# Optimization experiments

Measured on AMD Instinct MI355X. Metric: run time of the kernel, lower is better.

Reference implementation:

```python
import jax, jax.numpy as jnp
import numpy as np

B, S, D = 2, 512, 64

def setup_inputs() -> dict:
    key = jax.random.key(0)
    k1, k2, k3, k4, k5 = jax.random.split(key, 5)
    x = jax.random.normal(k1, (B, S, D, D), dtype=jnp.float32)
    log_A = jax.random.normal(k2, (D,), dtype=jnp.float32) * 0.02
    # nn.Linear(dim, 1): weight (1, dim) -> store as (dim,), bias scalar
    dt_w = jax.random.normal(k3, (D,), dtype=jnp.float32) * (1.0 / np.sqrt(D))
    dt_b = jax.random.normal(k4, (), dtype=jnp.float32) * (1.0 / np.sqrt(D))
    # LayerNorm over normalized_shape=(dim, dim)
    ln_w = jnp.ones((D, D), dtype=jnp.float32)
    ln_b = jnp.zeros((D, D), dtype=jnp.float32)
    return {"x": x, "log_A": log_A, "dt_w": dt_w, "dt_b": dt_b, "ln_w": ln_w, "ln_b": ln_b}

def _layernorm_2d(x, w, b, eps=1e-5):
    # normalize over last two dims (d, d)
    mu = jnp.mean(x, axis=(-2, -1), keepdims=True)
    var = jnp.var(x, axis=(-2, -1), keepdims=True)
    return (x - mu) * jax.lax.rsqrt(var + eps) * w + b

def reference(x, log_A, dt_w, dt_b, ln_w, ln_b):
    b, seq, d, _ = x.shape
    x_in = x
    xn = _layernorm_2d(x, ln_w, ln_b)                      # (b, s, d, d)
    A_cont = -jnp.exp(log_A)                               # (d,)
    dt = jax.nn.softplus(jnp.einsum('bsdc,c->bsd', xn, dt_w) + dt_b)  # (b, s, d)
    log_A_dt = dt * A_cont                                 # (b, s, d)
    cs = jnp.cumsum(log_A_dt, axis=1)                      # (b, s, d)
    log_M = cs[:, :, None, :] - cs[:, None, :, :]          # (b, t, j, d)
    idx = jnp.arange(seq)
    mask = (idx[:, None] >= idx[None, :])[None, :, :, None]  # causal (1, t, j, 1)
    M = jnp.exp(jnp.where(mask, log_M, -jnp.inf))          # (b, t, j, d)
    out = jnp.einsum('btjr,bjrc->btrc', M, xn)             # (b, t, d, d)
    return out + x_in
```

## Files before the change

### kernel.cpp

```cpp
#include <hip/hip_runtime.h>
#include <math.h>

#define BB 2
#define SS 512
#define DD 64
#define DDDD 4096
#define NC 32
#define CL (SS / NC)

__global__ __launch_bounds__(256) void k1_stats(
    const float* __restrict__ x, const float* __restrict__ log_A,
    const float* __restrict__ dt_w, const float* __restrict__ dt_b,
    const float* __restrict__ ln_w, const float* __restrict__ ln_b,
    float* __restrict__ a_out, float2* __restrict__ stats)
{
    const int bs  = blockIdx.x;
    const int tid = threadIdx.x;

    const float4* xp4 = (const float4*)(x + (size_t)bs * DDDD + tid * 16);
    float4 v0 = xp4[0], v1 = xp4[1], v2 = xp4[2], v3 = xp4[3];

    float sum = (v0.x+v0.y+v0.z+v0.w) + (v1.x+v1.y+v1.z+v1.w)
              + (v2.x+v2.y+v2.z+v2.w) + (v3.x+v3.y+v3.z+v3.w);
    float sq  = (v0.x*v0.x+v0.y*v0.y+v0.z*v0.z+v0.w*v0.w)
              + (v1.x*v1.x+v1.y*v1.y+v1.z*v1.z+v1.w*v1.w)
              + (v2.x*v2.x+v2.y*v2.y+v2.z*v2.z+v2.w*v2.w)
              + (v3.x*v3.x+v3.y*v3.y+v3.z*v3.z+v3.w*v3.w);

    #pragma unroll
    for (int off = 32; off > 0; off >>= 1) {
        sum += __shfl_down(sum, off);
        sq  += __shfl_down(sq,  off);
    }
    __shared__ float s_sum[4], s_sq[4];
    const int wv = tid >> 6, ln = tid & 63;
    if (ln == 0) { s_sum[wv] = sum; s_sq[wv] = sq; }
    __syncthreads();
    const float tsum = s_sum[0] + s_sum[1] + s_sum[2] + s_sum[3];
    const float tsq  = s_sq[0]  + s_sq[1]  + s_sq[2]  + s_sq[3];
    const float mu   = tsum * (1.0f / DDDD);
    const float var  = tsq  * (1.0f / DDDD) - mu * mu;
    const float rstd = rsqrtf(var + 1e-5f);

    const float4* lw4 = (const float4*)(ln_w + tid * 16);
    const float4* lb4 = (const float4*)(ln_b + tid * 16);
    const float4* dw4 = (const float4*)(dt_w + (tid & 3) * 16);
    float p = 0.f;
    #define ACC4(vv, ii) { \
        float4 lw = lw4[ii], lb = lb4[ii], dw = dw4[ii];            \
        p = fmaf(fmaf((vv.x - mu) * rstd, lw.x, lb.x), dw.x, p);    \
        p = fmaf(fmaf((vv.y - mu) * rstd, lw.y, lb.y), dw.y, p);    \
        p = fmaf(fmaf((vv.z - mu) * rstd, lw.z, lb.z), dw.z, p);    \
        p = fmaf(fmaf((vv.w - mu) * rstd, lw.w, lb.w), dw.w, p);    \
    }
    ACC4(v0, 0); ACC4(v1, 1); ACC4(v2, 2); ACC4(v3, 3);
    #undef ACC4

    p += __shfl_xor(p, 1);
    p += __shfl_xor(p, 2);

    if ((tid & 3) == 0) {
        const int d = tid >> 2;
        float z = p + dt_b[0];
        float dt = (z > 20.f) ? z : log1pf(expf(z));
        float la = dt * (-expf(log_A[d]));
        a_out[bs * DD + d] = expf(la);
    }
    if (tid == 0) stats[bs] = make_float2(mu, rstd);
}

__global__ __launch_bounds__(256) void k2a_partial(
    const float* __restrict__ x, const float* __restrict__ a_in,
    const float* __restrict__ ln_w, const float* __restrict__ ln_b,
    const float2* __restrict__ stats,
    float* __restrict__ Fbuf, float* __restrict__ Pbuf)
{
    const int gw = blockIdx.x * 4 + (threadIdx.x >> 6);
    const int c  = threadIdx.x & 63;
    const int ch = gw & (NC - 1);
    const int br = gw >> 5;
    const int b  = br >> 6, r = br & 63;

    const float lnw = ln_w[r * DD + c];
    const float lnb = ln_b[r * DD + c];

    const int t0 = ch * CL;
    const float*  xp = x + (((size_t)(b * SS + t0)) * DD + r) * DD + c;
    const float*  ap = a_in + (b * SS + t0) * DD + r;
    const float2* sp = stats + b * SS + t0;

    float state = 0.f, P = 1.f;
    #pragma unroll
    for (int t = 0; t < CL; t += 8) {
        float xv[8], av[8]; float2 st[8];
        #pragma unroll
        for (int i = 0; i < 8; ++i) {
            xv[i] = xp[(size_t)(t + i) * DDDD];
            av[i] = ap[(t + i) * DD];
            st[i] = sp[t + i];
        }
        #pragma unroll
        for (int i = 0; i < 8; ++i) {
            float xn = fmaf((xv[i] - st[i].x) * st[i].y, lnw, lnb);
            state = fmaf(av[i], state, xn);
            P *= av[i];
        }
    }
    Fbuf[(size_t)gw * DD + c] = state;
    if (c == 0) Pbuf[gw] = P;
}

__global__ __launch_bounds__(256) void k2b_final(
    const float* __restrict__ x, const float* __restrict__ a_in,
    const float* __restrict__ ln_w, const float* __restrict__ ln_b,
    const float2* __restrict__ stats,
    const float* __restrict__ Fbuf, const float* __restrict__ Pbuf,
    float* __restrict__ out)
{
    const int gw = blockIdx.x * 4 + (threadIdx.x >> 6);
    const int c  = threadIdx.x & 63;
    const int ch = gw & (NC - 1);
    const int br = gw >> 5;
    const int b  = br >> 6, r = br & 63;

    float carry = 0.f;
    {
        float f[NC], p[NC];
        #pragma unroll
        for (int v = 0; v < NC; ++v) {
            f[v] = Fbuf[(size_t)(br * NC + v) * DD + c];
            p[v] = Pbuf[br * NC + v];
        }
        #pragma unroll
        for (int v = 0; v < NC; ++v) {
            float pv = (v < ch) ? p[v] : 1.f;
            float fv = (v < ch) ? f[v] : 0.f;
            carry = fmaf(pv, carry, fv);
        }
    }

    const float lnw = ln_w[r * DD + c];
    const float lnb = ln_b[r * DD + c];

    const int t0 = ch * CL;
    const size_t xoff = (((size_t)(b * SS + t0)) * DD + r) * DD + c;
    const float*  xp = x + xoff;
    const float*  ap = a_in + (b * SS + t0) * DD + r;
    const float2* sp = stats + b * SS + t0;
    float* op = out + xoff;

    float state = carry;
    #pragma unroll
    for (int t = 0; t < CL; t += 8) {
        float xv[8], av[8]; float2 st[8];
        #pragma unroll
        for (int i = 0; i < 8; ++i) {
            xv[i] = xp[(size_t)(t + i) * DDDD];
            av[i] = ap[(t + i) * DD];
            st[i] = sp[t + i];
        }
        #pragma unroll
        for (int i = 0; i < 8; ++i) {
            float xn = fmaf((xv[i] - st[i].x) * st[i].y, lnw, lnb);
            state = fmaf(av[i], state, xn);
            op[(size_t)(t + i) * DDDD] = state + xv[i];
        }
    }
}

extern "C" void kernel_launch(void* const* d_in, const int* in_sizes, int n_in,
                              void* d_out, int out_size, void* d_ws, size_t ws_size,
                              hipStream_t stream) {
    const float* x     = (const float*)d_in[0];
    const float* log_A = (const float*)d_in[1];
    const float* dt_w  = (const float*)d_in[2];
    const float* dt_b  = (const float*)d_in[3];
    const float* ln_w  = (const float*)d_in[4];
    const float* ln_b  = (const float*)d_in[5];
    float* out = (float*)d_out;

    char* ws = (char*)d_ws;
    float*  a_buf = (float*)ws;
    float2* stats = (float2*)(ws + 262144);
    float*  Fbuf  = (float*)(ws + 262144 + 8192);
    float*  Pbuf  = (float*)(ws + 262144 + 8192 + 1048576);

    k1_stats<<<BB * SS, 256, 0, stream>>>(x, log_A, dt_w, dt_b, ln_w, ln_b, a_buf, stats);
    k2a_partial<<<BB * DD * NC / 4, 256, 0, stream>>>(x, a_buf, ln_w, ln_b, stats, Fbuf, Pbuf);
    k2b_final<<<BB * DD * NC / 4, 256, 0, stream>>>(x, a_buf, ln_w, ln_b, stats, Fbuf, Pbuf, out);
}
```

Baseline: 91.91 us.

## Fuse two-pass chunked scan into single pass with inter-block flag waits

Merges the partial-scan and final-scan kernels into one kernel. Each chunk keeps its x, normalized x and decay values in registers, publishes its chunk state and product behind a per-chunk flag, then spin-waits on the flags of earlier chunks before applying the carry and writing output. This drops the second full read of x and one kernel launch. In exchange it depends on forward-progress ordering of blocks to avoid deadlock, adds spin-wait latency along the chunk chain, and raises register pressure from the cached arrays. Flags are reset inside the stats kernel on every call.

```diff
diff --git a/kernel.cpp b/kernel.cpp
--- a/kernel.cpp
+++ b/kernel.cpp
@@ -12,10 +12,13 @@
     const float* __restrict__ x, const float* __restrict__ log_A,
     const float* __restrict__ dt_w, const float* __restrict__ dt_b,
     const float* __restrict__ ln_w, const float* __restrict__ ln_b,
-    float* __restrict__ a_out, float2* __restrict__ stats)
+    float* __restrict__ a_out, float2* __restrict__ stats,
+    unsigned int* __restrict__ flags)
 {
     const int bs  = blockIdx.x;
     const int tid = threadIdx.x;
+
+    if (tid < 4) flags[bs * 4 + tid] = 0u;
 
     const float4* xp4 = (const float4*)(x + (size_t)bs * DDDD + tid * 16);
     float4 v0 = xp4[0], v1 = xp4[1], v2 = xp4[2], v3 = xp4[3];
@@ -69,11 +72,13 @@
     if (tid == 0) stats[bs] = make_float2(mu, rstd);
 }
 
-__global__ __launch_bounds__(256) void k2a_partial(
+__global__ __launch_bounds__(256) void k2_scan1p(
     const float* __restrict__ x, const float* __restrict__ a_in,
     const float* __restrict__ ln_w, const float* __restrict__ ln_b,
     const float2* __restrict__ stats,
-    float* __restrict__ Fbuf, float* __restrict__ Pbuf)
+    float* __restrict__ Fbuf, float* __restrict__ Pbuf,
+    unsigned int* __restrict__ flags,
+    float* __restrict__ out)
 {
     const int gw = blockIdx.x * 4 + (threadIdx.x >> 6);
     const int c  = threadIdx.x & 63;
@@ -85,10 +90,12 @@
     const float lnb = ln_b[r * DD + c];
 
     const int t0 = ch * CL;
-    const float*  xp = x + (((size_t)(b * SS + t0)) * DD + r) * DD + c;
+    const size_t xoff = (((size_t)(b * SS + t0)) * DD + r) * DD + c;
+    const float*  xp = x + xoff;
     const float*  ap = a_in + (b * SS + t0) * DD + r;
     const float2* sp = stats + b * SS + t0;
 
+    float xvs[CL], xns[CL], as_[CL];
     float state = 0.f, P = 1.f;
     #pragma unroll
     for (int t = 0; t < CL; t += 8) {
@@ -104,67 +111,50 @@
             float xn = fmaf((xv[i] - st[i].x) * st[i].y, lnw, lnb);
             state = fmaf(av[i], state, xn);
             P *= av[i];
-        }
-    }
-    Fbuf[(size_t)gw * DD + c] = state;
-    if (c == 0) Pbuf[gw] = P;
-}
-
-__global__ __launch_bounds__(256) void k2b_final(
-    const float* __restrict__ x, const float* __restrict__ a_in,
-    const float* __restrict__ ln_w, const float* __restrict__ ln_b,
-    const float2* __restrict__ stats,
-    const float* __restrict__ Fbuf, const float* __restrict__ Pbuf,
-    float* __restrict__ out)
-{
-    const int gw = blockIdx.x * 4 + (threadIdx.x >> 6);
-    const int c  = threadIdx.x & 63;
-    const int ch = gw & (NC - 1);
-    const int br = gw >> 5;
-    const int b  = br >> 6, r = br & 63;
-
-    float carry = 0.f;
-    {
-        float f[NC], p[NC];
-        #pragma unroll
-        for (int v = 0; v < NC; ++v) {
-            f[v] = Fbuf[(size_t)(br * NC + v) * DD + c];
-            p[v] = Pbuf[br * NC + v];
-        }
-        #pragma unroll
-        for (int v = 0; v < NC; ++v) {
-            float pv = (v < ch) ? p[v] : 1.f;
-            float fv = (v < ch) ? f[v] : 0.f;
-            carry = fmaf(pv, carry, fv);
+            xvs[t + i] = xv[i];
+            xns[t + i] = xn;
+            as_[t + i] = av[i];
         }
     }
 
-    const float lnw = ln_w[r * DD + c];
-    const float lnb = ln_b[r * DD + c];
+    Fbuf[(size_t)gw * DD + c] = state;
+    if (c == 0) Pbuf[gw] = P;
+    __threadfence();
+    if (c == 0)
+        __hip_atomic_store(&flags[gw], 1u, __ATOMIC_RELAXED, __HIP_MEMORY_SCOPE_AGENT);
 
-    const int t0 = ch * CL;
-    const size_t xoff = (((size_t)(b * SS + t0)) * DD + r) * DD + c;
-    const float*  xp = x + xoff;
-    const float*  ap = a_in + (b * SS + t0) * DD + r;
-    const float2* sp = stats + b * SS + t0;
-    float* op = out + xoff;
+    if (c == 0) {
+        for (int v = 0; v < ch; ++v) {
+            while (__hip_atomic_load(&flags[br * NC + v], __ATOMIC_RELAXED,
+                                     __HIP_MEMORY_SCOPE_AGENT) == 0u) {
+                __builtin_amdgcn_s_sleep(2);
+            }
+        }
+    }
+    __threadfence();
 
-    float state = carry;
+    float carry = 0.f;
     #pragma unroll
-    for (int t = 0; t < CL; t += 8) {
-        float xv[8], av[8]; float2 st[8];
+    for (int vb = 0; vb < NC; vb += 8) {
+        float f[8], p[8];
         #pragma unroll
         for (int i = 0; i < 8; ++i) {
-            xv[i] = xp[(size_t)(t + i) * DDDD];
-            av[i] = ap[(t + i) * DD];
-            st[i] = sp[t + i];
+            f[i] = Fbuf[(size_t)(br * NC + vb + i) * DD + c];
+            p[i] = Pbuf[br * NC + vb + i];
         }
         #pragma unroll
         for (int i = 0; i < 8; ++i) {
-            float xn = fmaf((xv[i] - st[i].x) * st[i].y, lnw, lnb);
-            state = fmaf(av[i], state, xn);
-            op[(size_t)(t + i) * DDDD] = state + xv[i];
+            const int v = vb + i;
+            carry = fmaf((v < ch) ? p[i] : 1.f, carry, (v < ch) ? f[i] : 0.f);
         }
+    }
+
+    float st = carry;
+    float* op = out + xoff;
+    #pragma unroll
+    for (int t = 0; t < CL; ++t) {
+        st = fmaf(as_[t], st, xns[t]);
+        op[(size_t)t * DDDD] = st + xvs[t];
     }
 }
 
@@ -180,12 +170,14 @@
     float* out = (float*)d_out;
 
     char* ws = (char*)d_ws;
-    float*  a_buf = (float*)ws;
-    float2* stats = (float2*)(ws + 262144);
-    float*  Fbuf  = (float*)(ws + 262144 + 8192);
-    float*  Pbuf  = (float*)(ws + 262144 + 8192 + 1048576);
+    float*        a_buf = (float*)ws;
+    float2*       stats = (float2*)(ws + 262144);
+    float*        Fbuf  = (float*)(ws + 270336);
+    float*        Pbuf  = (float*)(ws + 270336 + 1048576);
+    unsigned int* flags = (unsigned int*)(ws + 270336 + 1048576 + 16384);
 
-    k1_stats<<<BB * SS, 256, 0, stream>>>(x, log_A, dt_w, dt_b, ln_w, ln_b, a_buf, stats);
-    k2a_partial<<<BB * DD * NC / 4, 256, 0, stream>>>(x, a_buf, ln_w, ln_b, stats, Fbuf, Pbuf);
-    k2b_final<<<BB * DD * NC / 4, 256, 0, stream>>>(x, a_buf, ln_w, ln_b, stats, Fbuf, Pbuf, out);
+    k1_stats<<<BB * SS, 256, 0, stream>>>(x, log_A, dt_w, dt_b, ln_w, ln_b,
+                                          a_buf, stats, flags);
+    k2_scan1p<<<BB * DD * NC / 4, 256, 0, stream>>>(x, a_buf, ln_w, ln_b, stats,
+                                                    Fbuf, Pbuf, flags, out);
 }
```

Result: slower. 336.2 us (+265.8%).
